# Performance work log

Hardware: AMD Instinct MI355X
Metric: run time of the kernel (lower is better)

Reference implementation:

```python
import jax, jax.numpy as jnp
import numpy as np

H = 512   # hidden_size
V = 5000  # output_size (vocab)
B = 128   # batch
S = 64    # encoder source length
T = 52    # max_trajectory_length


def setup_inputs() -> dict:
    key = jax.random.key(0)
    ks = jax.random.split(key, 16)
    sc = 0.05
    rn = lambda k, shape: jax.random.normal(k, shape, dtype=jnp.float32) * sc
    return dict(
        encoder_outputs=jax.random.normal(ks[0], (B, S, H), dtype=jnp.float32),
        h0=jax.random.normal(ks[1], (1, B, H), dtype=jnp.float32),
        c0=jax.random.normal(ks[2], (1, B, H), dtype=jnp.float32),
        target_tensor=jax.random.randint(ks[3], (B, T), 0, V),
        emb=rn(ks[4], (V, H)),
        Wa=rn(ks[5], (H, H)), ba=jnp.zeros((H,), jnp.float32),
        Ua=rn(ks[6], (H, H)), bu=jnp.zeros((H,), jnp.float32),
        Va=rn(ks[7], (H,)), bv=jnp.zeros((), jnp.float32),
        W_ih=rn(ks[8], (4 * H, 2 * H)), W_hh=rn(ks[9], (4 * H, H)),
        b_ih=jnp.zeros((4 * H,), jnp.float32), b_hh=jnp.zeros((4 * H,), jnp.float32),
        Wout=rn(ks[10], (V, H)), bout=jnp.zeros((V,), jnp.float32),
    )


def reference(encoder_outputs, h0, c0, target_tensor, emb,
              Wa, ba, Ua, bu, Va, bv,
              W_ih, W_hh, b_ih, b_hh, Wout, bout):
    # Dropout is identity in eval mode.
    b = target_tensor.shape[0]
    # Ua(keys) is constant across decode steps -> precompute once. [B,S,H]
    keys_proj = jnp.einsum('bsh,kh->bsk', encoder_outputs, Ua) + bu
    # Teacher forcing: input at step i is target[:, i-1], step 0 is token 0.
    tokens = jnp.concatenate(
        [jnp.zeros((b, 1), target_tensor.dtype), target_tensor[:, :-1]], axis=1)  # [B,T]

    def step(carry, tok):
        h, c = carry                                # [B,H] each
        x = emb[tok]                                # embedding lookup [B,H]
        q = h @ Wa.T + ba                           # Wa(query) [B,H]
        scores = jnp.tanh(q[:, None, :] + keys_proj) @ Va + bv  # [B,S]
        w = jax.nn.softmax(scores, axis=-1)         # attn weights [B,S]
        ctx = jnp.einsum('bs,bsh->bh', w, encoder_outputs)       # context [B,H]
        xi = jnp.concatenate([x, ctx], axis=-1)     # [B,2H]
        gates = xi @ W_ih.T + b_ih + h @ W_hh.T + b_hh           # [B,4H]
        i_g, f_g, g_g, o_g = jnp.split(gates, 4, axis=-1)        # torch gate order i,f,g,o
        c = jax.nn.sigmoid(f_g) * c + jax.nn.sigmoid(i_g) * jnp.tanh(g_g)
        h = jax.nn.sigmoid(o_g) * jnp.tanh(c)
        logits = h @ Wout.T + bout                  # [B,V]
        return (h, c), (logits, w)

    (h, c), (logits, attn) = jax.lax.scan(step, (h0[0], c0[0]), tokens.T)
    logits = jnp.transpose(logits, (1, 0, 2))       # [B,T,V]
    log_probs = jax.nn.log_softmax(logits, axis=-1)
    attn = jnp.transpose(attn, (1, 0, 2))           # [B,T,S]
    return log_probs, (h[None], c[None]), attn
```

## Files before the change

### kernel.cpp

```cpp
#include <hip/hip_runtime.h>
#include <math.h>

#define H 512
#define V 5000
#define BB 128
#define SS 64
#define TT 52
#define GSZ 16
#define NBLK 128
#define LROWS 96

typedef __attribute__((ext_vector_type(8))) short bf16x8;
typedef __attribute__((ext_vector_type(4))) float f32x4;
typedef __attribute__((ext_vector_type(2))) float f32x2;

__device__ __forceinline__ unsigned short f2b(float f) {
    unsigned u = __float_as_uint(f);
    return (unsigned short)((u + 0x7fffu + ((u >> 16) & 1u)) >> 16);
}
__device__ __forceinline__ float b2f(unsigned short u) {
    return __uint_as_float((unsigned)u << 16);
}
__device__ __forceinline__ float ftanh(float x) {
    return 1.f - 2.f / (1.f + __expf(2.f * x));
}
__device__ __forceinline__ float fsig(float x) {
    return 1.f / (1.f + __expf(-x));
}
__device__ __forceinline__ unsigned char f2fp8(float f) {
    return (unsigned char)__builtin_amdgcn_cvt_pk_fp8_f32(f, f, 0, 0);
}

__device__ __forceinline__ void pollf(unsigned* a, unsigned s)
{
    for (;;) {
        unsigned v;
        asm volatile("global_load_dword %0, %1, off sc0 sc1\n\ts_waitcnt vmcnt(0)"
                     : "=v"(v) : "v"(a) : "memory");
        if (v >= s) break;
        __builtin_amdgcn_s_sleep(1);
    }
}
__device__ __forceinline__ void fst(unsigned* p, unsigned v)
{
    asm volatile("global_store_dword %0, %1, off sc0 sc1" :: "v"(p), "v"(v) : "memory");
}
__device__ __forceinline__ void cstf4(float* p, f32x4 v)
{
    asm volatile("global_store_dwordx4 %0, %1, off sc0 sc1" :: "v"(p), "v"(v) : "memory");
}
__device__ __forceinline__ void cld4x16B(const unsigned short* p0, const unsigned short* p1,
                                         const unsigned short* p2, const unsigned short* p3,
                                         uint4& a, uint4& b, uint4& c, uint4& d)
{
    asm volatile(
        "global_load_dwordx4 %0, %4, off sc0 sc1\n\t"
        "global_load_dwordx4 %1, %5, off sc0 sc1\n\t"
        "global_load_dwordx4 %2, %6, off sc0 sc1\n\t"
        "global_load_dwordx4 %3, %7, off sc0 sc1\n\t"
        "s_waitcnt vmcnt(0)"
        : "=v"(a), "=v"(b), "=v"(c), "=v"(d)
        : "v"(p0), "v"(p1), "v"(p2), "v"(p3) : "memory");
}
__device__ __forceinline__ void cldf2(const float* p0, const float* p1, float& a, float& b)
{
    asm volatile(
        "global_load_dword %0, %2, off sc0 sc1\n\t"
        "global_load_dword %1, %3, off sc0 sc1\n\t"
        "s_waitcnt vmcnt(0)"
        : "=v"(a), "=v"(b) : "v"(p0), "v"(p1) : "memory");
}
__device__ __forceinline__ void cldf8s(const float* p, float* r)
{
    asm volatile(
        "global_load_dword %0, %8, off sc0 sc1\n\t"
        "global_load_dword %1, %8, off offset:64 sc0 sc1\n\t"
        "global_load_dword %2, %8, off offset:128 sc0 sc1\n\t"
        "global_load_dword %3, %8, off offset:192 sc0 sc1\n\t"
        "global_load_dword %4, %8, off offset:256 sc0 sc1\n\t"
        "global_load_dword %5, %8, off offset:320 sc0 sc1\n\t"
        "global_load_dword %6, %8, off offset:384 sc0 sc1\n\t"
        "global_load_dword %7, %8, off offset:448 sc0 sc1\n\t"
        "s_waitcnt vmcnt(0)"
        : "=v"(r[0]), "=v"(r[1]), "=v"(r[2]), "=v"(r[3]),
          "=v"(r[4]), "=v"(r[5]), "=v"(r[6]), "=v"(r[7])
        : "v"(p) : "memory");
}
__device__ __forceinline__ void cstu32c(unsigned* p, unsigned v)
{
    asm volatile("global_store_dword %0, %1, off sc0 sc1" :: "v"(p), "v"(v) : "memory");
}

__global__ __launch_bounds__(256)
void prep_w(const float* __restrict__ Wa, const float* __restrict__ Whh,
            const float* __restrict__ Wih,
            const float* __restrict__ ba, const float* __restrict__ bih,
            const float* __restrict__ bhh,
            const float* __restrict__ Ua, const float* __restrict__ Wout,
            const float* __restrict__ enc,
            unsigned short* __restrict__ Whb, unsigned short* __restrict__ Wxb,
            unsigned short* __restrict__ Wc,
            unsigned short* __restrict__ Uab, unsigned short* __restrict__ Woutb,
            unsigned short* __restrict__ encb, float* __restrict__ bbig)
{
    const int stride = gridDim.x * blockDim.x;
    const int t0 = blockIdx.x * blockDim.x + threadIdx.x;
    for (int idx = t0; idx < 2560 * 512; idx += stride) {
        const int j = idx >> 9, k = idx & 511;
        Whb[idx] = f2b((j < H) ? Wa[j * H + k] : Whh[(j - H) * H + k]);
    }
    for (int idx = t0; idx < 2048 * 512; idx += stride) {
        const int n = idx >> 9, k = idx & 511;
        Wxb[idx] = f2b(Wih[n * 2 * H + k]);
        Wc[idx]  = f2b(Wih[n * 2 * H + H + k]);
    }
    for (int idx = t0; idx < 512 * 512; idx += stride)   Uab[idx]   = f2b(Ua[idx]);
    for (int idx = t0; idx < V * 512; idx += stride)     Woutb[idx] = f2b(Wout[idx]);
    for (int idx = t0; idx < BB * SS * H; idx += stride) encb[idx]  = f2b(enc[idx]);
    for (int j = t0; j < 2560; j += stride)
        bbig[j] = (j < H) ? ba[j] : bih[j - H] + bhh[j - H];
}

__global__ __launch_bounds__(256)
void gather_x(const float* __restrict__ emb, const int* __restrict__ tgt,
              unsigned short* __restrict__ xall)
{
    const int stride = gridDim.x * blockDim.x;
    for (int idx = blockIdx.x * blockDim.x + threadIdx.x; idx < TT * BB * H; idx += stride) {
        const int k = idx & 511;
        const int row = idx >> 9;
        const int t = row >> 7, b = row & 127;
        const int tok = (t == 0) ? 0 : tgt[b * TT + t - 1];
        xall[idx] = f2b(emb[(size_t)tok * H + k]);
    }
}

template<int OUT_MODE, int PERMUTE>
__global__ __launch_bounds__(256, 2)
void gemm_mfma(const unsigned short* __restrict__ A,
               const unsigned short* __restrict__ B,
               const float* __restrict__ bias,
               float* __restrict__ Cf, unsigned short* __restrict__ Cb,
               unsigned char* __restrict__ C8,
               int M, int N)
{
    __shared__ unsigned short As[128][72];
    __shared__ unsigned short Bs[128][72];
    const int tid = threadIdx.x;
    const int m0 = blockIdx.y * 128, n0 = blockIdx.x * 128;
    const int lane = tid & 63, wv = tid >> 6;
    const int qm = (wv >> 1) * 64, qn = (wv & 1) * 64;
    const int fr = lane & 15, fg = lane >> 4;
    f32x4 acc[4][4];
#pragma unroll
    for (int i = 0; i < 4; ++i)
#pragma unroll
        for (int j = 0; j < 4; ++j) acc[i][j] = (f32x4){0.f, 0.f, 0.f, 0.f};

    const int srow = tid >> 3, sc = (tid & 7) * 8;
    for (int k0 = 0; k0 < H; k0 += 64) {
#pragma unroll
        for (int u = 0; u < 4; ++u) {
            const int row = srow + u * 32;
            *(uint4*)&As[row][sc] = *(const uint4*)&A[(size_t)(m0 + row) * H + k0 + sc];
            int nr = n0 + row; if (nr > N - 1) nr = N - 1;
            *(uint4*)&Bs[row][sc] = *(const uint4*)&B[(size_t)nr * H + k0 + sc];
        }
        __syncthreads();
#pragma unroll
        for (int ks = 0; ks < 2; ++ks) {
            const int kk = ks * 32 + fg * 8;
            bf16x8 av[4], bv[4];
#pragma unroll
            for (int i = 0; i < 4; ++i) {
                av[i] = *(const bf16x8*)&As[qm + i * 16 + fr][kk];
                bv[i] = *(const bf16x8*)&Bs[qn + i * 16 + fr][kk];
            }
#pragma unroll
            for (int i = 0; i < 4; ++i)
#pragma unroll
                for (int j = 0; j < 4; ++j)
                    acc[i][j] = __builtin_amdgcn_mfma_f32_16x16x32_bf16(av[i], bv[j], acc[i][j], 0, 0, 0);
        }
        __syncthreads();
    }
#pragma unroll
    for (int i = 0; i < 4; ++i) {
        const int r0 = m0 + qm + i * 16 + fg * 4;
#pragma unroll
        for (int j = 0; j < 4; ++j) {
            const int col = n0 + qn + j * 16 + fr;
            if (col < N) {
                const float bi = bias ? bias[col] : 0.f;
#pragma unroll
                for (int v = 0; v < 4; ++v) {
                    const int r = r0 + v;
                    const float val = acc[i][j][v] + bi;
                    if (OUT_MODE == 1) Cb[(size_t)r * N + col] = f2b(val);
                    else if (OUT_MODE == 2) C8[(size_t)r * N + col] = f2fp8(val);
                    else {
                        const size_t orow = PERMUTE ? ((size_t)(r & (BB - 1)) * TT + (r >> 7))
                                                    : (size_t)r;
                        Cf[orow * (size_t)N + col] = val;
                    }
                }
            }
        }
    }
}

struct PParams {
    const float* h0;
    const float* c0;
    const unsigned short* keysb;
    const unsigned char* encW8;
    const float* Va;
    const float* bv;
    const float* bbig;
    const unsigned short* Whb;
    const unsigned short* xgates;
    unsigned short* hbuf;
    float* Ybuf;
    unsigned short* hallb;
    float* attn;
    float* out_h;
    float* out_c;
    unsigned* hfl;
    unsigned* yfl;
};

__global__ __launch_bounds__(256, 1)
void persist(PParams p)
{
    __shared__ unsigned short WA[LROWS][520];
    __shared__ unsigned short h_s[16][520];
    __shared__ float qa_s[H];
    __shared__ float va_s[H];
    __shared__ float part[SS][4];
    __shared__ float wbuf[SS];
    __shared__ float gbuf[4 * H];
    __shared__ float cs[H];

    const int tid  = threadIdx.x;
    const int beta = blockIdx.x;
    const int grp  = beta & 7;
    const int slot = beta >> 3;
    const int gb   = grp * GSZ + slot;
    const int gi   = gb;
    const int wv   = tid >> 6, lane = tid & 63;
    const int fr   = lane & 15, fg = lane >> 4;

    unsigned short* hbg = p.hbuf + (size_t)grp * GSZ * H;
    float* ybg = p.Ybuf + (size_t)grp * 2560 * GSZ;

    for (int idx = tid; idx < LROWS * 64; idx += 256) {
        const int r = idx >> 6, c = idx & 63;
        *(uint4*)&WA[r][c * 8] =
            *(const uint4*)&p.Whb[((size_t)slot * 160 + r) * H + c * 8];
    }
    for (int j = tid; j < H; j += 256) {
        cs[j] = p.c0[(size_t)gb * H + j];
        va_s[j] = p.Va[j];
    }
    {
        const float* hp = p.h0 + (size_t)gb * H;
        const unsigned hp32 = (unsigned)f2b(hp[tid * 2]) |
                              ((unsigned)f2b(hp[tid * 2 + 1]) << 16);
        cstu32c((unsigned*)(hbg + (size_t)slot * H) + tid, hp32);
    }
    __syncthreads();
    if (tid == 0) fst(&p.hfl[gi * 32], 1u);

    for (int t = 0; t < TT; ++t) {
        const unsigned st = (unsigned)(t + 1);
        if (tid < GSZ) pollf(&p.hfl[(grp * GSZ + tid) * 32], st);
        __syncthreads();
        {
            uint4 a, b, c4, d;
            cld4x16B(hbg + (size_t)tid * 8, hbg + (size_t)(tid + 256) * 8,
                     hbg + (size_t)(tid + 512) * 8, hbg + (size_t)(tid + 768) * 8,
                     a, b, c4, d);
            const int r0 = tid >> 6, c0 = (tid & 63) * 8;
            *(uint4*)&h_s[r0][c0]      = a;
            *(uint4*)&h_s[r0 + 4][c0]  = b;
            *(uint4*)&h_s[r0 + 8][c0]  = c4;
            *(uint4*)&h_s[r0 + 12][c0] = d;
        }
        __syncthreads();
        for (int tt = wv; tt < 10; tt += 4) {
            const int jrow = slot * 160 + tt * 16 + fr;
            f32x4 acc = {0.f, 0.f, 0.f, 0.f};
            if (tt < 6) {
#pragma unroll
                for (int ks = 0; ks < 16; ++ks) {
                    bf16x8 A = *(const bf16x8*)&h_s[fr][ks * 32 + fg * 8];
                    bf16x8 B = *(const bf16x8*)&WA[tt * 16 + fr][ks * 32 + fg * 8];
                    acc = __builtin_amdgcn_mfma_f32_16x16x32_bf16(A, B, acc, 0, 0, 0);
                }
            } else {
                const unsigned short* wr = p.Whb + (size_t)jrow * H;
#pragma unroll
                for (int ks = 0; ks < 16; ++ks) {
                    bf16x8 A = *(const bf16x8*)&h_s[fr][ks * 32 + fg * 8];
                    bf16x8 B = *(const bf16x8*)&wr[ks * 32 + fg * 8];
                    acc = __builtin_amdgcn_mfma_f32_16x16x32_bf16(A, B, acc, 0, 0, 0);
                }
            }
            const float bb = p.bbig[jrow];
            f32x4 o;
#pragma unroll
            for (int i = 0; i < 4; ++i) o[i] = acc[i] + bb;
            cstf4(ybg + (size_t)jrow * GSZ + fg * 4, o);
        }
        __syncthreads();
        if (tid == 0) fst(&p.yfl[gi * 32], st);

        if (tid < 4) pollf(&p.yfl[(grp * GSZ + tid) * 32], st);
        __syncthreads();
        cldf2(ybg + (size_t)tid * GSZ + slot,
              ybg + (size_t)(tid + 256) * GSZ + slot,
              qa_s[tid], qa_s[tid + 256]);
        __syncthreads();
        {
            const int s = tid >> 2, q = tid & 3;
            const unsigned short* kp = p.keysb + ((size_t)gb * SS + s) * H + q * 128;
            const float* qp = qa_s + q * 128;
            const float* vp = va_s + q * 128;
            float a2 = 0.f, a2b = 0.f;
#pragma unroll
            for (int i8 = 0; i8 < 16; ++i8) {
                bf16x8 kv = *(const bf16x8*)&kp[i8 * 8];
#pragma unroll
                for (int u = 0; u < 8; u += 2) {
                    const int i = i8 * 8 + u;
                    a2  += ftanh(qp[i]     + b2f((unsigned short)kv[u]))     * vp[i];
                    a2b += ftanh(qp[i + 1] + b2f((unsigned short)kv[u + 1])) * vp[i + 1];
                }
            }
            part[s][q] = a2 + a2b;
        }
        __syncthreads();
        if (tid < 64) {
            float sc = part[tid][0] + part[tid][1] + part[tid][2] + part[tid][3] + p.bv[0];
            float m = sc;
            for (int o = 32; o; o >>= 1) m = fmaxf(m, __shfl_xor(m, o));
            const float e = __expf(sc - m);
            float ss = e;
            for (int o = 32; o; o >>= 1) ss += __shfl_xor(ss, o);
            const float w = e / ss;
            wbuf[tid] = w;
            p.attn[((size_t)gb * TT + t) * SS + tid] = w;
        }
        __syncthreads();
        float gc[8] = {0.f, 0.f, 0.f, 0.f, 0.f, 0.f, 0.f, 0.f};
        {
            const unsigned char* ew = p.encW8 + (size_t)gb * SS * 2048 + tid * 8;
#pragma unroll 8
            for (int s2 = 0; s2 < SS; ++s2) {
                const float w2 = wbuf[s2];
                const uint2 u = *(const uint2*)(ew + (size_t)s2 * 2048);
                const f32x2 e01 = __builtin_amdgcn_cvt_pk_f32_fp8(u.x, 0);
                const f32x2 e23 = __builtin_amdgcn_cvt_pk_f32_fp8(u.x, 1);
                const f32x2 e45 = __builtin_amdgcn_cvt_pk_f32_fp8(u.y, 0);
                const f32x2 e67 = __builtin_amdgcn_cvt_pk_f32_fp8(u.y, 1);
                gc[0] += w2 * e01[0]; gc[1] += w2 * e01[1];
                gc[2] += w2 * e23[0]; gc[3] += w2 * e23[1];
                gc[4] += w2 * e45[0]; gc[5] += w2 * e45[1];
                gc[6] += w2 * e67[0]; gc[7] += w2 * e67[1];
            }
        }
        if (tid < GSZ) pollf(&p.yfl[(grp * GSZ + tid) * 32], st);
        __syncthreads();
        {
            float yg[8];
            cldf8s(ybg + (size_t)(512 + tid * 8) * GSZ + slot, yg);
            bf16x8 xg = *(const bf16x8*)&p.xgates[((size_t)t * BB + gb) * 2048 + tid * 8];
#pragma unroll
            for (int i = 0; i < 8; ++i)
                gbuf[tid * 8 + i] = gc[i] + yg[i] + b2f((unsigned short)xg[i]);
        }
        __syncthreads();
        {
            const int last = (t == TT - 1);
            unsigned hpack = 0;
            float hn2[2], cn2[2];
#pragma unroll
            for (int u = 0; u < 2; ++u) {
                const int j = tid * 2 + u;
                const float ig  = gbuf[j];
                const float fgt = gbuf[512 + j];
                const float gg  = gbuf[1024 + j];
                const float og  = gbuf[1536 + j];
                const float co  = cs[j];
                const float cn = fsig(fgt) * co + fsig(ig) * ftanh(gg);
                const float hn = fsig(og) * ftanh(cn);
                cs[j] = cn;
                hn2[u] = hn; cn2[u] = cn;
                hpack |= ((unsigned)f2b(hn)) << (16 * u);
            }
            cstu32c((unsigned*)(hbg + (size_t)slot * H) + tid, hpack);
            *(unsigned*)&p.hallb[((size_t)t * BB + gb) * H + tid * 2] = hpack;
            if (last) {
#pragma unroll
                for (int u = 0; u < 2; ++u) {
                    p.out_h[gb * H + tid * 2 + u] = hn2[u];
                    p.out_c[gb * H + tid * 2 + u] = cn2[u];
                }
            }
        }
        __syncthreads();
        if (tid == 0) fst(&p.hfl[gi * 32], st + 1);
    }
}

__global__ __launch_bounds__(256)
void logsoftmax_rows(float* __restrict__ P)
{
    __shared__ float red[256];
    float* p = P + (size_t)blockIdx.x * V;
    const int tid = threadIdx.x;
    float m = -1e30f;
    for (int i = tid; i < V; i += 256) m = fmaxf(m, p[i]);
    red[tid] = m; __syncthreads();
    for (int sft = 128; sft; sft >>= 1) {
        if (tid < sft) red[tid] = fmaxf(red[tid], red[tid + sft]);
        __syncthreads();
    }
    m = red[0]; __syncthreads();
    float ssum = 0.f;
    for (int i = tid; i < V; i += 256) ssum += __expf(p[i] - m);
    red[tid] = ssum; __syncthreads();
    for (int sft = 128; sft; sft >>= 1) {
        if (tid < sft) red[tid] += red[tid + sft];
        __syncthreads();
    }
    const float lse = m + __logf(red[0]);
    for (int i = tid; i < V; i += 256) p[i] -= lse;
}

extern "C" void kernel_launch(void* const* d_in, const int* in_sizes, int n_in,
                              void* d_out, int out_size, void* d_ws, size_t ws_size,
                              hipStream_t stream)
{
    (void)in_sizes; (void)n_in; (void)out_size; (void)ws_size;
    const float* enc  = (const float*)d_in[0];
    const float* h0   = (const float*)d_in[1];
    const float* c0   = (const float*)d_in[2];
    const int*   tgt  = (const int*)  d_in[3];
    const float* emb  = (const float*)d_in[4];
    const float* Wa   = (const float*)d_in[5];
    const float* ba   = (const float*)d_in[6];
    const float* Ua   = (const float*)d_in[7];
    const float* bu   = (const float*)d_in[8];
    const float* Va   = (const float*)d_in[9];
    const float* bv   = (const float*)d_in[10];
    const float* Wih  = (const float*)d_in[11];
    const float* Whh  = (const float*)d_in[12];
    const float* bih  = (const float*)d_in[13];
    const float* bhh  = (const float*)d_in[14];
    const float* Wout = (const float*)d_in[15];
    const float* bout = (const float*)d_in[16];

    float* ws = (float*)d_ws;
    float* bbig = ws;
    float* Ybuf = bbig + 2560;
    unsigned* flags = (unsigned*)(Ybuf + 327680);
    unsigned* hfl = flags;
    unsigned* yfl = flags + 4096;
    unsigned short* Whb   = (unsigned short*)(flags + 8192);
    unsigned short* Wxb   = Whb + 1310720;
    unsigned short* Wc    = Wxb + 1048576;
    unsigned short* Uab   = Wc + 1048576;
    unsigned short* Woutb = Uab + 262144;
    unsigned short* encb  = Woutb + 2560000;
    unsigned short* keysb = encb + 4194304;
    unsigned short* xall  = keysb + 4194304;
    unsigned short* xgates= xall + 3407872;
    unsigned short* hallb = xgates + 13631488;
    unsigned short* hbuf  = hallb + 3407872;
    unsigned char*  encW8 = (unsigned char*)(hbuf + 65536);

    float* out    = (float*)d_out;
    float* out_h  = out + (size_t)BB * TT * V;
    float* out_c  = out_h + BB * H;
    float* out_at = out_c + BB * H;

    hipMemsetAsync(flags, 0, 8192 * sizeof(unsigned), stream);

    prep_w<<<dim3(2048), dim3(256), 0, stream>>>(
        Wa, Whh, Wih, ba, bih, bhh, Ua, Wout, enc,
        Whb, Wxb, Wc, Uab, Woutb, encb, bbig);
    gather_x<<<dim3(512), dim3(256), 0, stream>>>(emb, tgt, xall);

    gemm_mfma<1, 0><<<dim3(4, 64), dim3(256), 0, stream>>>(
        encb, Uab, bu, nullptr, keysb, nullptr, BB * SS, H);
    gemm_mfma<2, 0><<<dim3(16, 64), dim3(256), 0, stream>>>(
        encb, Wc, nullptr, nullptr, nullptr, encW8, BB * SS, 2048);
    gemm_mfma<1, 0><<<dim3(16, 52), dim3(256), 0, stream>>>(
        xall, Wxb, nullptr, nullptr, xgates, nullptr, TT * BB, 2048);

    PParams pp;
    pp.h0 = h0; pp.c0 = c0; pp.keysb = keysb; pp.encW8 = encW8;
    pp.Va = Va; pp.bv = bv; pp.bbig = bbig;
    pp.Whb = Whb; pp.xgates = xgates;
    pp.hbuf = hbuf; pp.Ybuf = Ybuf; pp.hallb = hallb;
    pp.attn = out_at; pp.out_h = out_h; pp.out_c = out_c;
    pp.hfl = hfl; pp.yfl = yfl;
    persist<<<dim3(NBLK), dim3(256), 0, stream>>>(pp);

    gemm_mfma<0, 1><<<dim3(40, 52), dim3(256), 0, stream>>>(
        hallb, Woutb, bout, out, nullptr, nullptr, TT * BB, V);
    logsoftmax_rows<<<dim3(BB * TT), dim3(256), 0, stream>>>(out);
}
```

Baseline: 1.273 ms.

## Replace flag-synchronized grouped recurrence with independent per-batch blocks using FP8 weights

The persistent recurrent kernel is restructured so that each block owns one batch row and computes the full Wa/W_hh projection itself with 512 threads. This removes the cross-block flag polling and the global exchange buffers for h and the gate projections. The recurrent weights are repacked as FP8 in a k-major layout and read from global/L2 by every block at every step, using scalar FMA instead of MFMA. In exchange, much more weight traffic is repeated across blocks, and the recurrent weights lose precision, which adds accuracy risk.

New measurement: 2.751 ms. +116.1%, slower.

```diff
diff --git a/kernel.cpp b/kernel.cpp
--- a/kernel.cpp
+++ b/kernel.cpp
@@ -6,9 +6,6 @@
 #define BB 128
 #define SS 64
 #define TT 52
-#define GSZ 16
-#define NBLK 128
-#define LROWS 96
 
 typedef __attribute__((ext_vector_type(8))) short bf16x8;
 typedef __attribute__((ext_vector_type(4))) float f32x4;
@@ -29,66 +26,6 @@
 }
 __device__ __forceinline__ unsigned char f2fp8(float f) {
     return (unsigned char)__builtin_amdgcn_cvt_pk_fp8_f32(f, f, 0, 0);
-}
-
-__device__ __forceinline__ void pollf(unsigned* a, unsigned s)
-{
-    for (;;) {
-        unsigned v;
-        asm volatile("global_load_dword %0, %1, off sc0 sc1\n\ts_waitcnt vmcnt(0)"
-                     : "=v"(v) : "v"(a) : "memory");
-        if (v >= s) break;
-        __builtin_amdgcn_s_sleep(1);
-    }
-}
-__device__ __forceinline__ void fst(unsigned* p, unsigned v)
-{
-    asm volatile("global_store_dword %0, %1, off sc0 sc1" :: "v"(p), "v"(v) : "memory");
-}
-__device__ __forceinline__ void cstf4(float* p, f32x4 v)
-{
-    asm volatile("global_store_dwordx4 %0, %1, off sc0 sc1" :: "v"(p), "v"(v) : "memory");
-}
-__device__ __forceinline__ void cld4x16B(const unsigned short* p0, const unsigned short* p1,
-                                         const unsigned short* p2, const unsigned short* p3,
-                                         uint4& a, uint4& b, uint4& c, uint4& d)
-{
-    asm volatile(
-        "global_load_dwordx4 %0, %4, off sc0 sc1\n\t"
-        "global_load_dwordx4 %1, %5, off sc0 sc1\n\t"
-        "global_load_dwordx4 %2, %6, off sc0 sc1\n\t"
-        "global_load_dwordx4 %3, %7, off sc0 sc1\n\t"
-        "s_waitcnt vmcnt(0)"
-        : "=v"(a), "=v"(b), "=v"(c), "=v"(d)
-        : "v"(p0), "v"(p1), "v"(p2), "v"(p3) : "memory");
-}
-__device__ __forceinline__ void cldf2(const float* p0, const float* p1, float& a, float& b)
-{
-    asm volatile(
-        "global_load_dword %0, %2, off sc0 sc1\n\t"
-        "global_load_dword %1, %3, off sc0 sc1\n\t"
-        "s_waitcnt vmcnt(0)"
-        : "=v"(a), "=v"(b) : "v"(p0), "v"(p1) : "memory");
-}
-__device__ __forceinline__ void cldf8s(const float* p, float* r)
-{
-    asm volatile(
-        "global_load_dword %0, %8, off sc0 sc1\n\t"
-        "global_load_dword %1, %8, off offset:64 sc0 sc1\n\t"
-        "global_load_dword %2, %8, off offset:128 sc0 sc1\n\t"
-        "global_load_dword %3, %8, off offset:192 sc0 sc1\n\t"
-        "global_load_dword %4, %8, off offset:256 sc0 sc1\n\t"
-        "global_load_dword %5, %8, off offset:320 sc0 sc1\n\t"
-        "global_load_dword %6, %8, off offset:384 sc0 sc1\n\t"
-        "global_load_dword %7, %8, off offset:448 sc0 sc1\n\t"
-        "s_waitcnt vmcnt(0)"
-        : "=v"(r[0]), "=v"(r[1]), "=v"(r[2]), "=v"(r[3]),
-          "=v"(r[4]), "=v"(r[5]), "=v"(r[6]), "=v"(r[7])
-        : "v"(p) : "memory");
-}
-__device__ __forceinline__ void cstu32c(unsigned* p, unsigned v)
-{
-    asm volatile("global_store_dword %0, %1, off sc0 sc1" :: "v"(p), "v"(v) : "memory");
 }
 
 __global__ __launch_bounds__(256)
@@ -98,16 +35,29 @@
             const float* __restrict__ bhh,
             const float* __restrict__ Ua, const float* __restrict__ Wout,
             const float* __restrict__ enc,
-            unsigned short* __restrict__ Whb, unsigned short* __restrict__ Wxb,
+            unsigned* __restrict__ WT8p, unsigned short* __restrict__ Wxb,
             unsigned short* __restrict__ Wc,
             unsigned short* __restrict__ Uab, unsigned short* __restrict__ Woutb,
             unsigned short* __restrict__ encb, float* __restrict__ bbig)
 {
     const int stride = gridDim.x * blockDim.x;
     const int t0 = blockIdx.x * blockDim.x + threadIdx.x;
-    for (int idx = t0; idx < 2560 * 512; idx += stride) {
-        const int j = idx >> 9, k = idx & 511;
-        Whb[idx] = f2b((j < H) ? Wa[j * H + k] : Whh[(j - H) * H + k]);
+    for (int idx = t0; idx < 128 * 2560; idx += stride) {
+        const int k4 = idx / 2560;
+        const int j  = idx - k4 * 2560;
+        const int k  = k4 * 4;
+        float w0, w1, w2, w3;
+        if (j < H) {
+            w0 = Wa[j * H + k];     w1 = Wa[j * H + k + 1];
+            w2 = Wa[j * H + k + 2]; w3 = Wa[j * H + k + 3];
+        } else {
+            const int n = j - H;
+            w0 = Whh[n * H + k];     w1 = Whh[n * H + k + 1];
+            w2 = Whh[n * H + k + 2]; w3 = Whh[n * H + k + 3];
+        }
+        unsigned v = __builtin_amdgcn_cvt_pk_fp8_f32(w0, w1, 0u, 0);
+        v = __builtin_amdgcn_cvt_pk_fp8_f32(w2, w3, v, 1);
+        WT8p[idx] = v;
     }
     for (int idx = t0; idx < 2048 * 512; idx += stride) {
         const int n = idx >> 9, k = idx & 511;
@@ -217,118 +167,75 @@
     const float* Va;
     const float* bv;
     const float* bbig;
-    const unsigned short* Whb;
+    const unsigned* WT8p;
     const unsigned short* xgates;
-    unsigned short* hbuf;
-    float* Ybuf;
     unsigned short* hallb;
     float* attn;
     float* out_h;
     float* out_c;
-    unsigned* hfl;
-    unsigned* yfl;
 };
 
-__global__ __launch_bounds__(256, 1)
+__global__ __launch_bounds__(512, 1)
 void persist(PParams p)
 {
-    __shared__ unsigned short WA[LROWS][520];
-    __shared__ unsigned short h_s[16][520];
-    __shared__ float qa_s[H];
-    __shared__ float va_s[H];
-    __shared__ float part[SS][4];
+    __shared__ float h_s[512];
+    __shared__ float cs[512];
+    __shared__ float va_s[512];
+    __shared__ float ybuf[2560];
+    __shared__ float part[SS][8];
     __shared__ float wbuf[SS];
-    __shared__ float gbuf[4 * H];
-    __shared__ float cs[H];
-
-    const int tid  = threadIdx.x;
-    const int beta = blockIdx.x;
-    const int grp  = beta & 7;
-    const int slot = beta >> 3;
-    const int gb   = grp * GSZ + slot;
-    const int gi   = gb;
-    const int wv   = tid >> 6, lane = tid & 63;
-    const int fr   = lane & 15, fg = lane >> 4;
-
-    unsigned short* hbg = p.hbuf + (size_t)grp * GSZ * H;
-    float* ybg = p.Ybuf + (size_t)grp * 2560 * GSZ;
-
-    for (int idx = tid; idx < LROWS * 64; idx += 256) {
-        const int r = idx >> 6, c = idx & 63;
-        *(uint4*)&WA[r][c * 8] =
-            *(const uint4*)&p.Whb[((size_t)slot * 160 + r) * H + c * 8];
-    }
-    for (int j = tid; j < H; j += 256) {
-        cs[j] = p.c0[(size_t)gb * H + j];
-        va_s[j] = p.Va[j];
-    }
-    {
-        const float* hp = p.h0 + (size_t)gb * H;
-        const unsigned hp32 = (unsigned)f2b(hp[tid * 2]) |
-                              ((unsigned)f2b(hp[tid * 2 + 1]) << 16);
-        cstu32c((unsigned*)(hbg + (size_t)slot * H) + tid, hp32);
-    }
+    __shared__ float gbuf[2048];
+
+    const int tid = threadIdx.x;
+    const int gb  = blockIdx.x;
+
+    h_s[tid]  = p.h0[(size_t)gb * H + tid];
+    cs[tid]   = p.c0[(size_t)gb * H + tid];
+    va_s[tid] = p.Va[tid];
     __syncthreads();
-    if (tid == 0) fst(&p.hfl[gi * 32], 1u);
 
     for (int t = 0; t < TT; ++t) {
-        const unsigned st = (unsigned)(t + 1);
-        if (tid < GSZ) pollf(&p.hfl[(grp * GSZ + tid) * 32], st);
-        __syncthreads();
         {
-            uint4 a, b, c4, d;
-            cld4x16B(hbg + (size_t)tid * 8, hbg + (size_t)(tid + 256) * 8,
-                     hbg + (size_t)(tid + 512) * 8, hbg + (size_t)(tid + 768) * 8,
-                     a, b, c4, d);
-            const int r0 = tid >> 6, c0 = (tid & 63) * 8;
-            *(uint4*)&h_s[r0][c0]      = a;
-            *(uint4*)&h_s[r0 + 4][c0]  = b;
-            *(uint4*)&h_s[r0 + 8][c0]  = c4;
-            *(uint4*)&h_s[r0 + 12][c0] = d;
-        }
-        __syncthreads();
-        for (int tt = wv; tt < 10; tt += 4) {
-            const int jrow = slot * 160 + tt * 16 + fr;
-            f32x4 acc = {0.f, 0.f, 0.f, 0.f};
-            if (tt < 6) {
-#pragma unroll
-                for (int ks = 0; ks < 16; ++ks) {
-                    bf16x8 A = *(const bf16x8*)&h_s[fr][ks * 32 + fg * 8];
-                    bf16x8 B = *(const bf16x8*)&WA[tt * 16 + fr][ks * 32 + fg * 8];
-                    acc = __builtin_amdgcn_mfma_f32_16x16x32_bf16(A, B, acc, 0, 0, 0);
-                }
-            } else {
-                const unsigned short* wr = p.Whb + (size_t)jrow * H;
-#pragma unroll
-                for (int ks = 0; ks < 16; ++ks) {
-                    bf16x8 A = *(const bf16x8*)&h_s[fr][ks * 32 + fg * 8];
-                    bf16x8 B = *(const bf16x8*)&wr[ks * 32 + fg * 8];
-                    acc = __builtin_amdgcn_mfma_f32_16x16x32_bf16(A, B, acc, 0, 0, 0);
-                }
-            }
-            const float bb = p.bbig[jrow];
-            f32x4 o;
-#pragma unroll
-            for (int i = 0; i < 4; ++i) o[i] = acc[i] + bb;
-            cstf4(ybg + (size_t)jrow * GSZ + fg * 4, o);
-        }
-        __syncthreads();
-        if (tid == 0) fst(&p.yfl[gi * 32], st);
-
-        if (tid < 4) pollf(&p.yfl[(grp * GSZ + tid) * 32], st);
-        __syncthreads();
-        cldf2(ybg + (size_t)tid * GSZ + slot,
-              ybg + (size_t)(tid + 256) * GSZ + slot,
-              qa_s[tid], qa_s[tid + 256]);
-        __syncthreads();
+            f32x2 ac0 = {0.f, 0.f}, ac1 = {0.f, 0.f}, ac2 = {0.f, 0.f},
+                  ac3 = {0.f, 0.f}, ac4 = {0.f, 0.f};
+#pragma unroll 2
+            for (int k4 = 0; k4 < 128; ++k4) {
+                const f32x4 h4 = *(const f32x4*)&h_s[k4 * 4];
+                const f32x2 a01 = {h4[0], h4[1]};
+                const f32x2 a23 = {h4[2], h4[3]};
+                const unsigned* wk = p.WT8p + (size_t)k4 * 2560 + tid;
+                const unsigned w0 = wk[0];
+                const unsigned w1 = wk[512];
+                const unsigned w2 = wk[1024];
+                const unsigned w3 = wk[1536];
+                const unsigned w4 = wk[2048];
+                ac0 += a01 * __builtin_amdgcn_cvt_pk_f32_fp8(w0, 0);
+                ac0 += a23 * __builtin_amdgcn_cvt_pk_f32_fp8(w0, 1);
+                ac1 += a01 * __builtin_amdgcn_cvt_pk_f32_fp8(w1, 0);
+                ac1 += a23 * __builtin_amdgcn_cvt_pk_f32_fp8(w1, 1);
+                ac2 += a01 * __builtin_amdgcn_cvt_pk_f32_fp8(w2, 0);
+                ac2 += a23 * __builtin_amdgcn_cvt_pk_f32_fp8(w2, 1);
+                ac3 += a01 * __builtin_amdgcn_cvt_pk_f32_fp8(w3, 0);
+                ac3 += a23 * __builtin_amdgcn_cvt_pk_f32_fp8(w3, 1);
+                ac4 += a01 * __builtin_amdgcn_cvt_pk_f32_fp8(w4, 0);
+                ac4 += a23 * __builtin_amdgcn_cvt_pk_f32_fp8(w4, 1);
+            }
+            ybuf[tid]        = ac0[0] + ac0[1] + p.bbig[tid];
+            ybuf[512 + tid]  = ac1[0] + ac1[1] + p.bbig[512 + tid];
+            ybuf[1024 + tid] = ac2[0] + ac2[1] + p.bbig[1024 + tid];
+            ybuf[1536 + tid] = ac3[0] + ac3[1] + p.bbig[1536 + tid];
+            ybuf[2048 + tid] = ac4[0] + ac4[1] + p.bbig[2048 + tid];
+        }
+        __syncthreads();
+
         {
-            const int s = tid >> 2, q = tid & 3;
-            const unsigned short* kp = p.keysb + ((size_t)gb * SS + s) * H + q * 128;
-            const float* qp = qa_s + q * 128;
-            const float* vp = va_s + q * 128;
+            const int s = tid >> 3, q = tid & 7;
+            const unsigned short* kp = p.keysb + ((size_t)gb * SS + s) * H + q * 64;
+            const float* qp = ybuf + q * 64;
+            const float* vp = va_s + q * 64;
             float a2 = 0.f, a2b = 0.f;
 #pragma unroll
-            for (int i8 = 0; i8 < 16; ++i8) {
+            for (int i8 = 0; i8 < 8; ++i8) {
                 bf16x8 kv = *(const bf16x8*)&kp[i8 * 8];
 #pragma unroll
                 for (int u = 0; u < 8; u += 2) {
@@ -341,7 +248,9 @@
         }
         __syncthreads();
         if (tid < 64) {
-            float sc = part[tid][0] + part[tid][1] + part[tid][2] + part[tid][3] + p.bv[0];
+            float sc = part[tid][0] + part[tid][1] + part[tid][2] + part[tid][3]
+                     + part[tid][4] + part[tid][5] + part[tid][6] + part[tid][7]
+                     + p.bv[0];
             float m = sc;
             for (int o = 32; o; o >>= 1) m = fmaxf(m, __shfl_xor(m, o));
             const float e = __expf(sc - m);
@@ -352,64 +261,44 @@
             p.attn[((size_t)gb * TT + t) * SS + tid] = w;
         }
         __syncthreads();
-        float gc[8] = {0.f, 0.f, 0.f, 0.f, 0.f, 0.f, 0.f, 0.f};
+
         {
-            const unsigned char* ew = p.encW8 + (size_t)gb * SS * 2048 + tid * 8;
+            float gc0 = 0.f, gc1 = 0.f, gc2 = 0.f, gc3 = 0.f;
+            const unsigned char* ew = p.encW8 + (size_t)gb * SS * 2048 + tid * 4;
 #pragma unroll 8
             for (int s2 = 0; s2 < SS; ++s2) {
                 const float w2 = wbuf[s2];
-                const uint2 u = *(const uint2*)(ew + (size_t)s2 * 2048);
-                const f32x2 e01 = __builtin_amdgcn_cvt_pk_f32_fp8(u.x, 0);
-                const f32x2 e23 = __builtin_amdgcn_cvt_pk_f32_fp8(u.x, 1);
-                const f32x2 e45 = __builtin_amdgcn_cvt_pk_f32_fp8(u.y, 0);
-                const f32x2 e67 = __builtin_amdgcn_cvt_pk_f32_fp8(u.y, 1);
-                gc[0] += w2 * e01[0]; gc[1] += w2 * e01[1];
-                gc[2] += w2 * e23[0]; gc[3] += w2 * e23[1];
-                gc[4] += w2 * e45[0]; gc[5] += w2 * e45[1];
-                gc[6] += w2 * e67[0]; gc[7] += w2 * e67[1];
-            }
-        }
-        if (tid < GSZ) pollf(&p.yfl[(grp * GSZ + tid) * 32], st);
-        __syncthreads();
+                const unsigned u = *(const unsigned*)(ew + (size_t)s2 * 2048);
+                const f32x2 e01 = __builtin_amdgcn_cvt_pk_f32_fp8(u, 0);
+                const f32x2 e23 = __builtin_amdgcn_cvt_pk_f32_fp8(u, 1);
+                gc0 += w2 * e01[0]; gc1 += w2 * e01[1];
+                gc2 += w2 * e23[0]; gc3 += w2 * e23[1];
+            }
+            const uint2 xu = *(const uint2*)&p.xgates[((size_t)t * BB + gb) * 2048 + tid * 4];
+            gbuf[tid * 4 + 0] = gc0 + ybuf[512 + tid * 4 + 0] + b2f((unsigned short)(xu.x & 0xffffu));
+            gbuf[tid * 4 + 1] = gc1 + ybuf[512 + tid * 4 + 1] + b2f((unsigned short)(xu.x >> 16));
+            gbuf[tid * 4 + 2] = gc2 + ybuf[512 + tid * 4 + 2] + b2f((unsigned short)(xu.y & 0xffffu));
+            gbuf[tid * 4 + 3] = gc3 + ybuf[512 + tid * 4 + 3] + b2f((unsigned short)(xu.y >> 16));
+        }
+        __syncthreads();
+
         {
-            float yg[8];
-            cldf8s(ybg + (size_t)(512 + tid * 8) * GSZ + slot, yg);
-            bf16x8 xg = *(const bf16x8*)&p.xgates[((size_t)t * BB + gb) * 2048 + tid * 8];
-#pragma unroll
-            for (int i = 0; i < 8; ++i)
-                gbuf[tid * 8 + i] = gc[i] + yg[i] + b2f((unsigned short)xg[i]);
-        }
-        __syncthreads();
-        {
-            const int last = (t == TT - 1);
-            unsigned hpack = 0;
-            float hn2[2], cn2[2];
-#pragma unroll
-            for (int u = 0; u < 2; ++u) {
-                const int j = tid * 2 + u;
-                const float ig  = gbuf[j];
-                const float fgt = gbuf[512 + j];
-                const float gg  = gbuf[1024 + j];
-                const float og  = gbuf[1536 + j];
-                const float co  = cs[j];
-                const float cn = fsig(fgt) * co + fsig(ig) * ftanh(gg);
-                const float hn = fsig(og) * ftanh(cn);
-                cs[j] = cn;
-                hn2[u] = hn; cn2[u] = cn;
-                hpack |= ((unsigned)f2b(hn)) << (16 * u);
-            }
-            cstu32c((unsigned*)(hbg + (size_t)slot * H) + tid, hpack);
-            *(unsigned*)&p.hallb[((size_t)t * BB + gb) * H + tid * 2] = hpack;
-            if (last) {
-#pragma unroll
-                for (int u = 0; u < 2; ++u) {
-                    p.out_h[gb * H + tid * 2 + u] = hn2[u];
-                    p.out_c[gb * H + tid * 2 + u] = cn2[u];
-                }
-            }
-        }
-        __syncthreads();
-        if (tid == 0) fst(&p.hfl[gi * 32], st + 1);
+            const float ig  = gbuf[tid];
+            const float fgt = gbuf[512 + tid];
+            const float gg  = gbuf[1024 + tid];
+            const float og  = gbuf[1536 + tid];
+            const float co  = cs[tid];
+            const float cn = fsig(fgt) * co + fsig(ig) * ftanh(gg);
+            const float hn = fsig(og) * ftanh(cn);
+            cs[tid] = cn;
+            h_s[tid] = hn;
+            p.hallb[((size_t)t * BB + gb) * H + tid] = f2b(hn);
+            if (t == TT - 1) {
+                p.out_h[(size_t)gb * H + tid] = hn;
+                p.out_c[(size_t)gb * H + tid] = cn;
+            }
+        }
+        __syncthreads();
     }
 }
 
@@ -463,12 +352,8 @@
 
     float* ws = (float*)d_ws;
     float* bbig = ws;
-    float* Ybuf = bbig + 2560;
-    unsigned* flags = (unsigned*)(Ybuf + 327680);
-    unsigned* hfl = flags;
-    unsigned* yfl = flags + 4096;
-    unsigned short* Whb   = (unsigned short*)(flags + 8192);
-    unsigned short* Wxb   = Whb + 1310720;
+    unsigned* WT8p = (unsigned*)(bbig + 2560);
+    unsigned short* Wxb   = (unsigned short*)(WT8p + 327680);
     unsigned short* Wc    = Wxb + 1048576;
     unsigned short* Uab   = Wc + 1048576;
     unsigned short* Woutb = Uab + 262144;
@@ -477,19 +362,16 @@
     unsigned short* xall  = keysb + 4194304;
     unsigned short* xgates= xall + 3407872;
     unsigned short* hallb = xgates + 13631488;
-    unsigned short* hbuf  = hallb + 3407872;
-    unsigned char*  encW8 = (unsigned char*)(hbuf + 65536);
+    unsigned char*  encW8 = (unsigned char*)(hallb + 3407872);
 
     float* out    = (float*)d_out;
     float* out_h  = out + (size_t)BB * TT * V;
     float* out_c  = out_h + BB * H;
     float* out_at = out_c + BB * H;
 
-    hipMemsetAsync(flags, 0, 8192 * sizeof(unsigned), stream);
-
     prep_w<<<dim3(2048), dim3(256), 0, stream>>>(
         Wa, Whh, Wih, ba, bih, bhh, Ua, Wout, enc,
-        Whb, Wxb, Wc, Uab, Woutb, encb, bbig);
+        WT8p, Wxb, Wc, Uab, Woutb, encb, bbig);
     gather_x<<<dim3(512), dim3(256), 0, stream>>>(emb, tgt, xall);
 
     gemm_mfma<1, 0><<<dim3(4, 64), dim3(256), 0, stream>>>(
@@ -502,11 +384,10 @@
     PParams pp;
     pp.h0 = h0; pp.c0 = c0; pp.keysb = keysb; pp.encW8 = encW8;
     pp.Va = Va; pp.bv = bv; pp.bbig = bbig;
-    pp.Whb = Whb; pp.xgates = xgates;
-    pp.hbuf = hbuf; pp.Ybuf = Ybuf; pp.hallb = hallb;
+    pp.WT8p = WT8p; pp.xgates = xgates;
+    pp.hallb = hallb;
     pp.attn = out_at; pp.out_h = out_h; pp.out_c = out_c;
-    pp.hfl = hfl; pp.yfl = yfl;
-    persist<<<dim3(NBLK), dim3(256), 0, stream>>>(pp);
+    persist<<<dim3(BB), dim3(512), 0, stream>>>(pp);
 
     gemm_mfma<0, 1><<<dim3(40, 52), dim3(256), 0, stream>>>(
         hallb, Woutb, bout, out, nullptr, nullptr, TT * BB, V);
```
